# Kernel tuning notes

Hardware: AMD Instinct MI355X
Metric: run time of the kernel (lower is better)

## Reference

```python
import jax, jax.numpy as jnp
import numpy as np

VOXEL_SIZE = np.array([0.2, 0.2, 4.0], dtype=np.float32)
PC_MIN = np.array([0.0, -40.0, -3.0], dtype=np.float32)
BN_EPS = 1e-3
N_POINTS = 1_500_000
N_VOXELS = 200_000
C_IN = 7   # (4 - 3) + 6 stats channels (cluster offset + voxel-center offset)
C_OUT = 64


def setup_inputs() -> dict:
    key = jax.random.key(0)
    ks = jax.random.split(key, 8)
    features = jax.random.normal(ks[0], (N_POINTS, 4), dtype=jnp.float32)
    point2voxel = jax.random.randint(ks[1], (N_POINTS,), 0, N_VOXELS).astype(jnp.int32)
    voxel_coors = jnp.stack([
        jax.random.randint(ks[2], (N_VOXELS,), 0, 2),    # batch idx
        jnp.zeros((N_VOXELS,), jnp.int32),               # z (pillars -> 0)
        jax.random.randint(ks[3], (N_VOXELS,), 0, 400),  # y bin
        jax.random.randint(ks[4], (N_VOXELS,), 0, 352),  # x bin
    ], axis=1).astype(jnp.int32)
    W = jax.random.normal(ks[5], (C_IN, C_OUT), dtype=jnp.float32) * 0.1
    bn_gamma = jnp.ones((C_OUT,), jnp.float32)
    bn_beta = jnp.zeros((C_OUT,), jnp.float32)
    bn_mean = jax.random.normal(ks[6], (C_OUT,), dtype=jnp.float32) * 0.01
    bn_var = jax.random.uniform(ks[7], (C_OUT,), minval=0.5, maxval=1.5, dtype=jnp.float32)
    return dict(features=features, W=W, bn_gamma=bn_gamma, bn_beta=bn_beta,
                bn_mean=bn_mean, bn_var=bn_var, point2voxel=point2voxel,
                voxel_coors=voxel_coors)


def reference(features, W, bn_gamma, bn_beta, bn_mean, bn_var, point2voxel, voxel_coors):
    M = voxel_coors.shape[0]
    xyz = features[:, :3]

    # --- stats: cluster-center offset (per-voxel mean of xyz, mapped back) ---
    cnt = jax.ops.segment_sum(jnp.ones((xyz.shape[0],), xyz.dtype), point2voxel,
                              num_segments=M)
    vmean = jax.ops.segment_sum(xyz, point2voxel, num_segments=M)
    vmean = vmean / jnp.maximum(cnt, 1.0)[:, None]
    cluster_off = xyz - vmean[point2voxel]

    # --- stats: voxel-center offset ---
    vs = jnp.asarray(VOXEL_SIZE)
    mn = jnp.asarray(PC_MIN)
    # coors layout is (batch, z, y, x) -> take (x, y, z)
    centers = (voxel_coors[:, jnp.array([3, 2, 1])].astype(jnp.float32) + 0.5) * vs + mn
    center_off = xyz - centers[point2voxel]

    feats = jnp.concatenate([cluster_off, center_off, features[:, 3:]], axis=-1)  # [N,7]

    # --- PFN layer: Linear(bias=False) + BN1d (eval stats) + ReLU ---
    h = feats @ W
    h = (h - bn_mean) * jax.lax.rsqrt(bn_var + BN_EPS) * bn_gamma + bn_beta
    h = jax.nn.relu(h)

    # --- scatter max-reduce to voxels ---
    vfeats = jax.ops.segment_max(h, point2voxel, num_segments=M)
    vfeats = jnp.where(jnp.isfinite(vfeats), vfeats, 0.0)  # guard rare empty voxels
    return vfeats, voxel_coors
```

## Files before the change

kernel.cpp:

```cpp
#include <hip/hip_runtime.h>


#define BBITS  8
#define BVOX   (1 << BBITS)
#define QVOX   64
#define PCAP   768
#define GT     256
#define NRR    9
#define NBBITS 7
#define NBLK   (1 << NBBITS)
#define BMAX   800
#define SCH    4096

__global__ __launch_bounds__(256) void hist_k(const int* __restrict__ p2v,
                                              int* __restrict__ mat,
                                              int N, int NBIN, int chunk) {
    __shared__ int h[BMAX];
    int b = blockIdx.x, tid = threadIdx.x;
    for (int k = tid; k < NBIN; k += 256) h[k] = 0;
    __syncthreads();
    int s = b * chunk, e = min(N, s + chunk);
    for (int i = s + tid; i < e; i += 256)
        atomicAdd(&h[p2v[i] >> BBITS], 1);
    __syncthreads();
    for (int k = tid; k < NBIN; k += 256) mat[b * NBIN + k] = h[k];
}

__global__ void scanA_k(int* __restrict__ mat, int* __restrict__ bsum,
                        int NBIN, int S) {
    __shared__ int s[256];
    int tid = threadIdx.x;
    int base = blockIdx.x * SCH + tid * 16;
    int idx[16], c[16];
    int tsum = 0;
#pragma unroll
    for (int j = 0; j < 16; ++j) {
        int p = base + j;
        if (p < S) {
            int g = p >> NBBITS, b = p & (NBLK - 1);
            idx[j] = b * NBIN + g;
            c[j] = mat[idx[j]];
        } else {
            idx[j] = -1;
            c[j] = 0;
        }
        tsum += c[j];
    }
    s[tid] = tsum;
    __syncthreads();
    for (int off = 1; off < 256; off <<= 1) {
        int v = (tid >= off) ? s[tid - off] : 0;
        __syncthreads();
        s[tid] += v;
        __syncthreads();
    }
    int run = s[tid] - tsum;
#pragma unroll
    for (int j = 0; j < 16; ++j) {
        if (idx[j] >= 0) mat[idx[j]] = run;
        run += c[j];
    }
    if (tid == 255) bsum[blockIdx.x] = s[255];
}

__global__ void scanB_k(int* __restrict__ bsum, int nb) {
    __shared__ int s[256];
    int tid = threadIdx.x;
    int v = (tid < nb) ? bsum[tid] : 0;
    s[tid] = v;
    __syncthreads();
    for (int off = 1; off < 256; off <<= 1) {
        int t = (tid >= off) ? s[tid - off] : 0;
        __syncthreads();
        s[tid] += t;
        __syncthreads();
    }
    if (tid < nb) bsum[tid] = s[tid] - v;
}

__global__ __launch_bounds__(512) void scatter_pay_k(
    const int* __restrict__ p2v, const float4* __restrict__ feats,
    const int* __restrict__ mat, const int* __restrict__ bsum,
    float4* __restrict__ pay, unsigned char* __restrict__ voxid,
    int N, int NBIN, int chunk) {
    __shared__ int cur[BMAX];
    int b = blockIdx.x, tid = threadIdx.x;
    for (int g = tid; g < NBIN; g += 512)
        cur[g] = mat[b * NBIN + g] + bsum[((g << NBBITS) | b) >> 12];
    __syncthreads();
    int s = b * chunk, e = min(N, s + chunk);
    for (int i = s + tid; i < e; i += 512) {
        int v = p2v[i];
        int g = v >> BBITS;
        int pos = atomicAdd(&cur[g], 1);
        pay[pos] = feats[i];
        voxid[pos] = (unsigned char)(v & (BVOX - 1));
    }
}

__global__ __launch_bounds__(256, 8) void gather_quarter_k(
    const float4* __restrict__ pay, const unsigned char* __restrict__ voxid,
    const int* __restrict__ mat, const int* __restrict__ bsum,
    const float* __restrict__ W,
    const float* __restrict__ gamma, const float* __restrict__ beta,
    const float* __restrict__ mean, const float* __restrict__ var,
    const int* __restrict__ coors,
    float* __restrict__ out_v, float* __restrict__ out_c,
    int M, int NBIN, int N) {
    __shared__ float4 s_pay[PCAP];
    __shared__ int    s_cnt[QVOX];
    __shared__ int    s_cur[QVOX];
    __shared__ float  s_cx[QVOX], s_cy[QVOX], s_cz[QVOX];

    int bk = blockIdx.x, tid = threadIdx.x;
    int lane = tid & 63, w = tid >> 6;
    int g = bk >> 2, h = bk & 3;

    float w0 = W[0 * 64 + lane], w1 = W[1 * 64 + lane], w2 = W[2 * 64 + lane];
    float w3 = W[3 * 64 + lane], w4 = W[4 * 64 + lane], w5 = W[5 * 64 + lane];
    float w6 = W[6 * 64 + lane];
    float sc = gamma[lane] * rsqrtf(var[lane] + 1e-3f);
    float bi = beta[lane] - mean[lane] * sc;
    float sgn = (sc >= 0.0f) ? 1.0f : -1.0f;
    float u0 = sgn * (w0 + w3), u1 = sgn * (w1 + w4);
    float u2 = sgn * (w2 + w5), u3 = sgn * w6;

    int s = mat[g] + bsum[(g << NBBITS) >> 12];
    int e = (g + 1 < NBIN) ? (mat[g + 1] + bsum[((g + 1) << NBBITS) >> 12]) : N;
    int L = min(e - s, GT * NRR);

    int vx[NRR];
#pragma unroll
    for (int r = 0; r < NRR; ++r) {
        int j = tid + r * GT;
        int x = (j < L) ? (int)voxid[s + j] : -1;
        vx[r] = (x >= 0 && (x >> 6) == h) ? (x & (QVOX - 1)) : -1;
    }
    if (tid < QVOX) s_cnt[tid] = 0;
    __syncthreads();
#pragma unroll
    for (int r = 0; r < NRR; ++r)
        if (vx[r] >= 0) atomicAdd(&s_cnt[vx[r]], 1);

    int vbase = bk << 6;
    if (tid < QVOX) {
        int vg = vbase + tid;
        if (vg < M) {
            int4 cc = ((const int4*)coors)[vg];
            ((float4*)out_c)[vg] = make_float4((float)cc.x, (float)cc.y,
                                               (float)cc.z, (float)cc.w);
            s_cx[tid] = (cc.w + 0.5f) * 0.2f;
            s_cy[tid] = (cc.z + 0.5f) * 0.2f - 40.0f;
            s_cz[tid] = (cc.y + 0.5f) * 4.0f - 3.0f;
        }
    }
    __syncthreads();

    if (w == 0) {
        int c = s_cnt[lane];
        int x = c;
        for (int off = 1; off < 64; off <<= 1) {
            int y = __shfl_up(x, off);
            if (lane >= off) x += y;
        }
        s_cur[lane] = x - c;
    }
    __syncthreads();

#pragma unroll
    for (int r = 0; r < NRR; ++r)
        if (vx[r] >= 0) {
            int pos = atomicAdd(&s_cur[vx[r]], 1);
            float4 f = pay[s + tid + r * GT];
            if (pos < PCAP) s_pay[pos] = f;
        }
    __syncthreads();

    int lv0 = w << 4;
    int cnts[16];
#pragma unroll
    for (int q = 0; q < 16; ++q) cnts[q] = s_cnt[lv0 + q];
    int st = (lv0 == 0) ? 0 : s_cur[lv0 - 1];

    for (int q = 0; q < 16; ++q) {
        int lv = lv0 + q;
        int v = vbase + lv;
        int npts = cnts[q];
        float cenx = s_cx[lv], ceny = s_cy[lv], cenz = s_cz[lv];
        float sx = 0.f, sy = 0.f, sz = 0.f;
        float amax = -3.402823466e+38f;
        int i = 0;
        for (; i + 3 < npts; i += 4) {
            float4 f0 = s_pay[st + i + 0];
            float4 f1 = s_pay[st + i + 1];
            float4 f2 = s_pay[st + i + 2];
            float4 f3 = s_pay[st + i + 3];
            sx += f0.x + f1.x + f2.x + f3.x;
            sy += f0.y + f1.y + f2.y + f3.y;
            sz += f0.z + f1.z + f2.z + f3.z;
            float a0 = f0.x * u0 + f0.y * u1 + f0.z * u2 + f0.w * u3;
            float a1 = f1.x * u0 + f1.y * u1 + f1.z * u2 + f1.w * u3;
            float a2 = f2.x * u0 + f2.y * u1 + f2.z * u2 + f2.w * u3;
            float a3 = f3.x * u0 + f3.y * u1 + f3.z * u2 + f3.w * u3;
            amax = fmaxf(fmaxf(fmaxf(amax, a0), fmaxf(a1, a2)), a3);
        }
        for (; i < npts; ++i) {
            float4 f = s_pay[st + i];
            sx += f.x; sy += f.y; sz += f.z;
            float a = f.x * u0 + f.y * u1 + f.z * u2 + f.w * u3;
            amax = fmaxf(amax, a);
        }
        float res = 0.0f;
        if (npts > 0) {
            float inv = 1.0f / (float)npts;
            float mx = sx * inv, my = sy * inv, mz = sz * inv;
            float K = mx * w0 + my * w1 + mz * w2 +
                      cenx * w3 + ceny * w4 + cenz * w5;
            float aext = sgn * amax;
            res = fmaxf((aext - K) * sc + bi, 0.0f);
        }
        if (v < M) out_v[(size_t)v * 64 + lane] = res;
        st += npts;
    }
}

extern "C" void kernel_launch(void* const* d_in, const int* in_sizes, int n_in,
                              void* d_out, int out_size, void* d_ws, size_t ws_size,
                              hipStream_t stream) {
    const float* features = (const float*)d_in[0];
    const float* W        = (const float*)d_in[1];
    const float* gamma    = (const float*)d_in[2];
    const float* beta     = (const float*)d_in[3];
    const float* mean     = (const float*)d_in[4];
    const float* var      = (const float*)d_in[5];
    const int*   p2v      = (const int*)d_in[6];
    const int*   coors    = (const int*)d_in[7];
    int N = in_sizes[0] / 4;
    int M = in_sizes[7] / 4;

    int NBIN = (M + BVOX - 1) >> BBITS;
    int S = NBIN * NBLK;
    int chunk = (N + NBLK - 1) / NBLK;

    float4* pay           = (float4*)d_ws;
    unsigned char* voxid  = (unsigned char*)(pay + N);
    int* mat              = (int*)(voxid + ((N + 3) & ~3));
    int* bsum             = mat + S;

    float* out_v = (float*)d_out;
    float* out_c = out_v + (size_t)M * 64;

    hist_k<<<NBLK, 256, 0, stream>>>(p2v, mat, N, NBIN, chunk);
    int nbA = (S + SCH - 1) / SCH;
    scanA_k<<<nbA, 256, 0, stream>>>(mat, bsum, NBIN, S);
    scanB_k<<<1, 256, 0, stream>>>(bsum, nbA);
    scatter_pay_k<<<NBLK, 512, 0, stream>>>(
        p2v, (const float4*)features, mat, bsum, pay, voxid, N, NBIN, chunk);
    gather_quarter_k<<<NBIN * 4, GT, 0, stream>>>(
        pay, voxid, mat, bsum, W, gamma, beta, mean, var,
        coors, out_v, out_c, M, NBIN, N);
}
```

Measured before the change: 128.5 us.

## Gather per 512-voxel super-bin with 1024-thread blocks instead of quarter blocks

Doubles the bucket size to 512 voxels and stores the in-bin voxel id as a 16-bit value. One 1024-thread block now processes a whole super-bin, replacing four 256-thread blocks that each reread every voxel id in a 256-voxel bin and kept only their quarter. The goal is to read each point's metadata once and cut the number of bins the histogram and scatter kernels handle. In exchange, the grid has far fewer, larger blocks (about 391, each using roughly 67KB of LDS), so occupancy and load balance across CUs get worse. The intra-block prefix sum over 512 counters also becomes a multi-step shared-memory scan with many barriers.

Result: slower. 152.9 us (+19.0%).

```diff
diff --git a/kernel.cpp b/kernel.cpp
--- a/kernel.cpp
+++ b/kernel.cpp
@@ -1,33 +1,32 @@
 #include <hip/hip_runtime.h>
 
 
-#define BBITS  8
-#define BVOX   (1 << BBITS)
-#define QVOX   64
-#define PCAP   768
-#define GT     256
-#define NRR    9
+#define SBB    9
+#define SVOX   (1 << SBB)
+#define PCAP   4224
+#define GT     1024
+#define NR     5
 #define NBBITS 7
 #define NBLK   (1 << NBBITS)
-#define BMAX   800
+#define NSBMAX 400
 #define SCH    4096
 
 __global__ __launch_bounds__(256) void hist_k(const int* __restrict__ p2v,
                                               int* __restrict__ mat,
-                                              int N, int NBIN, int chunk) {
-    __shared__ int h[BMAX];
+                                              int N, int NSB, int chunk) {
+    __shared__ int h[NSBMAX];
     int b = blockIdx.x, tid = threadIdx.x;
-    for (int k = tid; k < NBIN; k += 256) h[k] = 0;
+    for (int k = tid; k < NSB; k += 256) h[k] = 0;
     __syncthreads();
     int s = b * chunk, e = min(N, s + chunk);
     for (int i = s + tid; i < e; i += 256)
-        atomicAdd(&h[p2v[i] >> BBITS], 1);
-    __syncthreads();
-    for (int k = tid; k < NBIN; k += 256) mat[b * NBIN + k] = h[k];
+        atomicAdd(&h[p2v[i] >> SBB], 1);
+    __syncthreads();
+    for (int k = tid; k < NSB; k += 256) mat[b * NSB + k] = h[k];
 }
 
 __global__ void scanA_k(int* __restrict__ mat, int* __restrict__ bsum,
-                        int NBIN, int S) {
+                        int NSB, int S) {
     __shared__ int s[256];
     int tid = threadIdx.x;
     int base = blockIdx.x * SCH + tid * 16;
@@ -37,8 +36,8 @@
     for (int j = 0; j < 16; ++j) {
         int p = base + j;
         if (p < S) {
-            int g = p >> NBBITS, b = p & (NBLK - 1);
-            idx[j] = b * NBIN + g;
+            int sb = p >> NBBITS, b = p & (NBLK - 1);
+            idx[j] = b * NSB + sb;
             c[j] = mat[idx[j]];
         } else {
             idx[j] = -1;
@@ -78,43 +77,42 @@
     if (tid < nb) bsum[tid] = s[tid] - v;
 }
 
-__global__ __launch_bounds__(512) void scatter_pay_k(
+__global__ __launch_bounds__(512) void scatter1_k(
     const int* __restrict__ p2v, const float4* __restrict__ feats,
     const int* __restrict__ mat, const int* __restrict__ bsum,
-    float4* __restrict__ pay, unsigned char* __restrict__ voxid,
-    int N, int NBIN, int chunk) {
-    __shared__ int cur[BMAX];
+    float4* __restrict__ pay, unsigned short* __restrict__ aux,
+    int N, int NSB, int chunk) {
+    __shared__ int cur[NSBMAX];
     int b = blockIdx.x, tid = threadIdx.x;
-    for (int g = tid; g < NBIN; g += 512)
-        cur[g] = mat[b * NBIN + g] + bsum[((g << NBBITS) | b) >> 12];
+    for (int k = tid; k < NSB; k += 512)
+        cur[k] = mat[b * NSB + k] + bsum[((k << NBBITS) | b) >> 12];
     __syncthreads();
     int s = b * chunk, e = min(N, s + chunk);
     for (int i = s + tid; i < e; i += 512) {
         int v = p2v[i];
-        int g = v >> BBITS;
-        int pos = atomicAdd(&cur[g], 1);
+        int sb = v >> SBB;
+        int pos = atomicAdd(&cur[sb], 1);
         pay[pos] = feats[i];
-        voxid[pos] = (unsigned char)(v & (BVOX - 1));
-    }
-}
-
-__global__ __launch_bounds__(256, 8) void gather_quarter_k(
-    const float4* __restrict__ pay, const unsigned char* __restrict__ voxid,
+        aux[pos] = (unsigned short)(v & (SVOX - 1));
+    }
+}
+
+__global__ __launch_bounds__(1024, 8) void gather_sb_k(
+    const float4* __restrict__ pay, const unsigned short* __restrict__ aux,
     const int* __restrict__ mat, const int* __restrict__ bsum,
     const float* __restrict__ W,
     const float* __restrict__ gamma, const float* __restrict__ beta,
     const float* __restrict__ mean, const float* __restrict__ var,
     const int* __restrict__ coors,
     float* __restrict__ out_v, float* __restrict__ out_c,
-    int M, int NBIN, int N) {
+    int M, int NSB, int N) {
     __shared__ float4 s_pay[PCAP];
-    __shared__ int    s_cnt[QVOX];
-    __shared__ int    s_cur[QVOX];
-    __shared__ float  s_cx[QVOX], s_cy[QVOX], s_cz[QVOX];
-
-    int bk = blockIdx.x, tid = threadIdx.x;
+    __shared__ int    s_cnt[SVOX];
+    __shared__ int    s_cur[SVOX];
+    __shared__ float  s_cx[SVOX], s_cy[SVOX], s_cz[SVOX];
+
+    int sb = blockIdx.x, tid = threadIdx.x;
     int lane = tid & 63, w = tid >> 6;
-    int g = bk >> 2, h = bk & 3;
 
     float w0 = W[0 * 64 + lane], w1 = W[1 * 64 + lane], w2 = W[2 * 64 + lane];
     float w3 = W[3 * 64 + lane], w4 = W[4 * 64 + lane], w5 = W[5 * 64 + lane];
@@ -125,25 +123,25 @@
     float u0 = sgn * (w0 + w3), u1 = sgn * (w1 + w4);
     float u2 = sgn * (w2 + w5), u3 = sgn * w6;
 
-    int s = mat[g] + bsum[(g << NBBITS) >> 12];
-    int e = (g + 1 < NBIN) ? (mat[g + 1] + bsum[((g + 1) << NBBITS) >> 12]) : N;
-    int L = min(e - s, GT * NRR);
-
-    int vx[NRR];
-#pragma unroll
-    for (int r = 0; r < NRR; ++r) {
+    int s = mat[sb] + bsum[sb >> 5];
+    int e = (sb + 1 < NSB) ? (mat[sb + 1] + bsum[(sb + 1) >> 5]) : N;
+    int L = min(e - s, PCAP);
+
+    int vx[NR];
+#pragma unroll
+    for (int r = 0; r < NR; ++r) {
         int j = tid + r * GT;
-        int x = (j < L) ? (int)voxid[s + j] : -1;
-        vx[r] = (x >= 0 && (x >> 6) == h) ? (x & (QVOX - 1)) : -1;
-    }
-    if (tid < QVOX) s_cnt[tid] = 0;
-    __syncthreads();
-#pragma unroll
-    for (int r = 0; r < NRR; ++r)
+        vx[r] = (j < L) ? (int)aux[s + j] : -1;
+    }
+
+    if (tid < SVOX) s_cnt[tid] = 0;
+    __syncthreads();
+#pragma unroll
+    for (int r = 0; r < NR; ++r)
         if (vx[r] >= 0) atomicAdd(&s_cnt[vx[r]], 1);
 
-    int vbase = bk << 6;
-    if (tid < QVOX) {
+    int vbase = sb << SBB;
+    if (tid < SVOX) {
         int vg = vbase + tid;
         if (vg < M) {
             int4 cc = ((const int4*)coors)[vg];
@@ -156,71 +154,78 @@
     }
     __syncthreads();
 
-    if (w == 0) {
-        int c = s_cnt[lane];
-        int x = c;
-        for (int off = 1; off < 64; off <<= 1) {
-            int y = __shfl_up(x, off);
-            if (lane >= off) x += y;
-        }
-        s_cur[lane] = x - c;
-    }
-    __syncthreads();
-
-#pragma unroll
-    for (int r = 0; r < NRR; ++r)
+    if (tid < SVOX) s_cur[tid] = s_cnt[tid];
+    __syncthreads();
+    for (int off = 1; off < SVOX; off <<= 1) {
+        int t = 0;
+        if (tid < SVOX && tid >= off) t = s_cur[tid - off];
+        __syncthreads();
+        if (tid < SVOX) s_cur[tid] += t;
+        __syncthreads();
+    }
+    int ex = 0;
+    if (tid < SVOX) ex = s_cur[tid] - s_cnt[tid];
+    __syncthreads();
+    if (tid < SVOX) s_cur[tid] = ex;
+    __syncthreads();
+
+#pragma unroll
+    for (int r = 0; r < NR; ++r)
         if (vx[r] >= 0) {
             int pos = atomicAdd(&s_cur[vx[r]], 1);
             float4 f = pay[s + tid + r * GT];
-            if (pos < PCAP) s_pay[pos] = f;
-        }
-    __syncthreads();
-
-    int lv0 = w << 4;
-    int cnts[16];
-#pragma unroll
-    for (int q = 0; q < 16; ++q) cnts[q] = s_cnt[lv0 + q];
+            s_pay[pos] = f;
+        }
+    __syncthreads();
+
+    int lv0 = w << 5;
     int st = (lv0 == 0) ? 0 : s_cur[lv0 - 1];
 
-    for (int q = 0; q < 16; ++q) {
-        int lv = lv0 + q;
-        int v = vbase + lv;
-        int npts = cnts[q];
-        float cenx = s_cx[lv], ceny = s_cy[lv], cenz = s_cz[lv];
-        float sx = 0.f, sy = 0.f, sz = 0.f;
-        float amax = -3.402823466e+38f;
-        int i = 0;
-        for (; i + 3 < npts; i += 4) {
-            float4 f0 = s_pay[st + i + 0];
-            float4 f1 = s_pay[st + i + 1];
-            float4 f2 = s_pay[st + i + 2];
-            float4 f3 = s_pay[st + i + 3];
-            sx += f0.x + f1.x + f2.x + f3.x;
-            sy += f0.y + f1.y + f2.y + f3.y;
-            sz += f0.z + f1.z + f2.z + f3.z;
-            float a0 = f0.x * u0 + f0.y * u1 + f0.z * u2 + f0.w * u3;
-            float a1 = f1.x * u0 + f1.y * u1 + f1.z * u2 + f1.w * u3;
-            float a2 = f2.x * u0 + f2.y * u1 + f2.z * u2 + f2.w * u3;
-            float a3 = f3.x * u0 + f3.y * u1 + f3.z * u2 + f3.w * u3;
-            amax = fmaxf(fmaxf(fmaxf(amax, a0), fmaxf(a1, a2)), a3);
-        }
-        for (; i < npts; ++i) {
-            float4 f = s_pay[st + i];
-            sx += f.x; sy += f.y; sz += f.z;
-            float a = f.x * u0 + f.y * u1 + f.z * u2 + f.w * u3;
-            amax = fmaxf(amax, a);
-        }
-        float res = 0.0f;
-        if (npts > 0) {
-            float inv = 1.0f / (float)npts;
-            float mx = sx * inv, my = sy * inv, mz = sz * inv;
-            float K = mx * w0 + my * w1 + mz * w2 +
-                      cenx * w3 + ceny * w4 + cenz * w5;
-            float aext = sgn * amax;
-            res = fmaxf((aext - K) * sc + bi, 0.0f);
-        }
-        if (v < M) out_v[(size_t)v * 64 + lane] = res;
-        st += npts;
+    for (int half = 0; half < 2; ++half) {
+        int vb16 = lv0 + half * 16;
+        int cnts[16];
+#pragma unroll
+        for (int q = 0; q < 16; ++q) cnts[q] = s_cnt[vb16 + q];
+        for (int q = 0; q < 16; ++q) {
+            int lv = vb16 + q;
+            int v = vbase + lv;
+            int npts = cnts[q];
+            float cenx = s_cx[lv], ceny = s_cy[lv], cenz = s_cz[lv];
+            float sx = 0.f, sy = 0.f, sz = 0.f;
+            float amax = -3.402823466e+38f;
+            int i = 0;
+            for (; i + 3 < npts; i += 4) {
+                float4 f0 = s_pay[st + i + 0];
+                float4 f1 = s_pay[st + i + 1];
+                float4 f2 = s_pay[st + i + 2];
+                float4 f3 = s_pay[st + i + 3];
+                sx += f0.x + f1.x + f2.x + f3.x;
+                sy += f0.y + f1.y + f2.y + f3.y;
+                sz += f0.z + f1.z + f2.z + f3.z;
+                float a0 = f0.x * u0 + f0.y * u1 + f0.z * u2 + f0.w * u3;
+                float a1 = f1.x * u0 + f1.y * u1 + f1.z * u2 + f1.w * u3;
+                float a2 = f2.x * u0 + f2.y * u1 + f2.z * u2 + f2.w * u3;
+                float a3 = f3.x * u0 + f3.y * u1 + f3.z * u2 + f3.w * u3;
+                amax = fmaxf(fmaxf(fmaxf(amax, a0), fmaxf(a1, a2)), a3);
+            }
+            for (; i < npts; ++i) {
+                float4 f = s_pay[st + i];
+                sx += f.x; sy += f.y; sz += f.z;
+                float a = f.x * u0 + f.y * u1 + f.z * u2 + f.w * u3;
+                amax = fmaxf(amax, a);
+            }
+            float res = 0.0f;
+            if (npts > 0) {
+                float inv = 1.0f / (float)npts;
+                float mx = sx * inv, my = sy * inv, mz = sz * inv;
+                float K = mx * w0 + my * w1 + mz * w2 +
+                          cenx * w3 + ceny * w4 + cenz * w5;
+                float aext = sgn * amax;
+                res = fmaxf((aext - K) * sc + bi, 0.0f);
+            }
+            if (v < M) out_v[(size_t)v * 64 + lane] = res;
+            st += npts;
+        }
     }
 }
 
@@ -238,25 +243,25 @@
     int N = in_sizes[0] / 4;
     int M = in_sizes[7] / 4;
 
-    int NBIN = (M + BVOX - 1) >> BBITS;
-    int S = NBIN * NBLK;
+    int NSB = (M + SVOX - 1) >> SBB;
+    int S = NSB * NBLK;
     int chunk = (N + NBLK - 1) / NBLK;
 
-    float4* pay           = (float4*)d_ws;
-    unsigned char* voxid  = (unsigned char*)(pay + N);
-    int* mat              = (int*)(voxid + ((N + 3) & ~3));
-    int* bsum             = mat + S;
+    float4* pay          = (float4*)d_ws;
+    unsigned short* aux  = (unsigned short*)(pay + N);
+    int* mat             = (int*)((char*)aux + (((size_t)N * 2 + 3) & ~(size_t)3));
+    int* bsum            = mat + S;
 
     float* out_v = (float*)d_out;
     float* out_c = out_v + (size_t)M * 64;
 
-    hist_k<<<NBLK, 256, 0, stream>>>(p2v, mat, N, NBIN, chunk);
+    hist_k<<<NBLK, 256, 0, stream>>>(p2v, mat, N, NSB, chunk);
     int nbA = (S + SCH - 1) / SCH;
-    scanA_k<<<nbA, 256, 0, stream>>>(mat, bsum, NBIN, S);
+    scanA_k<<<nbA, 256, 0, stream>>>(mat, bsum, NSB, S);
     scanB_k<<<1, 256, 0, stream>>>(bsum, nbA);
-    scatter_pay_k<<<NBLK, 512, 0, stream>>>(
-        p2v, (const float4*)features, mat, bsum, pay, voxid, N, NBIN, chunk);
-    gather_quarter_k<<<NBIN * 4, GT, 0, stream>>>(
-        pay, voxid, mat, bsum, W, gamma, beta, mean, var,
-        coors, out_v, out_c, M, NBIN, N);
-}
+    scatter1_k<<<NBLK, 512, 0, stream>>>(
+        p2v, (const float4*)features, mat, bsum, pay, aux, N, NSB, chunk);
+    gather_sb_k<<<NSB, GT, 0, stream>>>(
+        pay, aux, mat, bsum, W, gamma, beta, mean, var,
+        coors, out_v, out_c, M, NSB, N);
+}
```
